# Kernel tuning notes

Hardware: AMD Instinct MI355X
Metric: run time of the kernel (lower is better)

The kernel has to match this reference:

```python
import jax, jax.numpy as jnp
import numpy as np

N_NODES = 100000
N_EDGES = 1200000
D_FEAT = 64
D_OUT = 128


def setup_inputs() -> dict:
    key = jax.random.key(0)
    k1, k2, k3, k4, k5, k6 = jax.random.split(key, 6)
    hk = jax.random.normal(k1, (N_NODES, D_FEAT), dtype=jnp.float32)
    hu = jax.random.normal(k2, (N_NODES, D_FEAT), dtype=jnp.float32)
    W = jax.random.normal(k3, (D_OUT, D_FEAT), dtype=jnp.float32) * 0.05
    b = jax.random.normal(k4, (D_OUT,), dtype=jnp.float32) * 0.05
    src = jax.random.randint(k5, (N_EDGES,), 0, N_NODES, dtype=jnp.int64)
    dst = jax.random.randint(k6, (N_EDGES,), 0, N_NODES, dtype=jnp.int64)
    return {"hk": hk, "hu": hu, "W": W, "b": b, "src": src, "dst": dst}


def reference(hk, hu, W, b, src, dst):
    n = hk.shape[0]
    # u_dot_v: per-edge score = <hk[src], hu[dst]>  -> [E]
    scores = jnp.sum(hk[src] * hu[dst], axis=-1)
    # edge_softmax: softmax over edges grouped by destination node
    seg_max = jax.ops.segment_max(scores, dst, num_segments=n)  # [N]
    ex = jnp.exp(scores - seg_max[dst])                          # [E]
    seg_sum = jax.ops.segment_sum(ex, dst, num_segments=n)      # [N]
    alpha = ex / seg_sum[dst]                                    # [E]
    # u_mul_e_sum: weighted scatter-aggregate of source features into dst
    rst = jax.ops.segment_sum(hk[src] * alpha[:, None], dst, num_segments=n)  # [N, D]
    # fc + relu
    return jax.nn.relu(rst @ W.T + b)
```

## Files before the change

### kernel.cpp

```cpp
#include <hip/hip_runtime.h>
#include <math.h>

#define D_FEAT 64
#define D_OUT  128

__global__ void k_count(const int* __restrict__ dst, int* __restrict__ deg, int E) {
    int e = blockIdx.x * blockDim.x + threadIdx.x;
    if (e >= E) return;
    atomicAdd(deg + dst[e], 1);
}

__global__ __launch_bounds__(256) void k_scan_a(const int* __restrict__ deg,
                                                int* __restrict__ rowptr,
                                                int* __restrict__ partials, int N) {
    __shared__ int wsum[4];
    const int t = threadIdx.x;
    const int base = blockIdx.x * 1024 + t * 4;
    int v0 = (base + 0 < N) ? deg[base + 0] : 0;
    int v1 = (base + 1 < N) ? deg[base + 1] : 0;
    int v2 = (base + 2 < N) ? deg[base + 2] : 0;
    int v3 = (base + 3 < N) ? deg[base + 3] : 0;
    int lsum = v0 + v1 + v2 + v3;
    int x = lsum;
#pragma unroll
    for (int off = 1; off < 64; off <<= 1) {
        int y = __shfl_up(x, off);
        if ((t & 63) >= off) x += y;
    }
    const int wid = t >> 6;
    if ((t & 63) == 63) wsum[wid] = x;
    __syncthreads();
    int woff = 0;
    for (int w = 0; w < wid; ++w) woff += wsum[w];
    int run = woff + x - lsum;
    if (base + 0 < N) rowptr[base + 0] = run; run += v0;
    if (base + 1 < N) rowptr[base + 1] = run; run += v1;
    if (base + 2 < N) rowptr[base + 2] = run; run += v2;
    if (base + 3 < N) rowptr[base + 3] = run;
    if (t == 0) partials[blockIdx.x] = wsum[0] + wsum[1] + wsum[2] + wsum[3];
}

__global__ __launch_bounds__(128) void k_scan_b(int* __restrict__ partials, int NB) {
    __shared__ int buf[128];
    const int t = threadIdx.x;
    const int orig = (t < NB) ? partials[t] : 0;
    buf[t] = orig;
    __syncthreads();
#pragma unroll
    for (int off = 1; off < 128; off <<= 1) {
        int v = (t >= off) ? buf[t - off] : 0;
        __syncthreads();
        buf[t] += v;
        __syncthreads();
    }
    if (t < NB) partials[t] = buf[t] - orig;
}

__global__ __launch_bounds__(256) void k_scan_c(int* __restrict__ rowptr,
                                                int* __restrict__ cursor,
                                                const int* __restrict__ partials,
                                                int N, int E) {
    const int t = threadIdx.x;
    const int base = blockIdx.x * 1024 + t * 4;
    const int add = partials[blockIdx.x];
#pragma unroll
    for (int i = 0; i < 4; ++i) {
        if (base + i < N) {
            int v = rowptr[base + i] + add;
            rowptr[base + i] = v;
            cursor[base + i] = v;
        }
    }
    if (blockIdx.x == 0 && t == 0) rowptr[N] = E;
}

__global__ __launch_bounds__(256) void k_fill(const int* __restrict__ src,
                                              const int* __restrict__ dst,
                                              int* __restrict__ cursor,
                                              int* __restrict__ srcs,
                                              int E, int N) {
    const int pid = (int)(blockIdx.x & 7);
    const int cb  = (int)(blockIdx.x >> 3);
    const int cpp = (int)(gridDim.x >> 3);
    const int lo = (int)(((long long)pid * N) / 8);
    const int hi = (int)(((long long)(pid + 1) * N) / 8);

    const int nq = E >> 2;
    const int stride = cpp * 256;
    for (int q = cb * 256 + (int)threadIdx.x; q < nq; q += stride) {
        const int4 d4 = reinterpret_cast<const int4*>(dst)[q];
        const int e0 = q * 4;
        if (d4.x >= lo && d4.x < hi) { int pos = atomicAdd(cursor + d4.x, 1); srcs[pos] = src[e0 + 0]; }
        if (d4.y >= lo && d4.y < hi) { int pos = atomicAdd(cursor + d4.y, 1); srcs[pos] = src[e0 + 1]; }
        if (d4.z >= lo && d4.z < hi) { int pos = atomicAdd(cursor + d4.z, 1); srcs[pos] = src[e0 + 2]; }
        if (d4.w >= lo && d4.w < hi) { int pos = atomicAdd(cursor + d4.w, 1); srcs[pos] = src[e0 + 3]; }
    }
    if (cb == 0 && (int)threadIdx.x < (E & 3)) {
        int e = nq * 4 + (int)threadIdx.x;
        int d = dst[e];
        if (d >= lo && d < hi) { int pos = atomicAdd(cursor + d, 1); srcs[pos] = src[e]; }
    }
}

__global__ __launch_bounds__(256) void k_agg(const float* __restrict__ hk,
                                             const float* __restrict__ hu,
                                             const int* __restrict__ rowptr,
                                             const int* __restrict__ srcs,
                                             float* __restrict__ rst, int N) {
    const int tid = blockIdx.x * blockDim.x + threadIdx.x;
    const int n = tid >> 6;
    if (n >= N) return;
    const int lane = tid & 63;
    const int q = lane & 15;
    const int g = lane >> 4;

    const int beg = rowptr[n];
    const int end = rowptr[n + 1];

    const float4 hv = *reinterpret_cast<const float4*>(hu + (size_t)n * D_FEAT + q * 4);

    float s = 0.f;
    float4 acc = make_float4(0.f, 0.f, 0.f, 0.f);

    auto process = [&](const float4& a) {
        float dsc = a.x * hv.x + a.y * hv.y + a.z * hv.z + a.w * hv.w;
        dsc += __shfl_xor(dsc, 1);
        dsc += __shfl_xor(dsc, 2);
        dsc += __shfl_xor(dsc, 4);
        dsc += __shfl_xor(dsc, 8);
        const float pe = __expf(fmaxf(fminf(dsc, 80.f), -80.f));
        s += pe;
        acc.x += pe * a.x;
        acc.y += pe * a.y;
        acc.z += pe * a.z;
        acc.w += pe * a.w;
    };

    int p = beg + g;
    if (p < end) {
        float4 a = *reinterpret_cast<const float4*>(hk + (size_t)srcs[p] * D_FEAT + q * 4);
        for (p += 4; p < end; p += 4) {
            const float4 a2 = *reinterpret_cast<const float4*>(hk + (size_t)srcs[p] * D_FEAT + q * 4);
            process(a);
            a = a2;
        }
        process(a);
    }

#pragma unroll
    for (int off = 16; off <= 32; off <<= 1) {
        s     += __shfl_xor(s, off);
        acc.x += __shfl_xor(acc.x, off);
        acc.y += __shfl_xor(acc.y, off);
        acc.z += __shfl_xor(acc.z, off);
        acc.w += __shfl_xor(acc.w, off);
    }

    if (g == 0) {
        float4 o;
        if (end > beg) {
            const float inv = 1.f / s;
            o = make_float4(acc.x * inv, acc.y * inv, acc.z * inv, acc.w * inv);
        } else {
            o = make_float4(0.f, 0.f, 0.f, 0.f);
        }
        *reinterpret_cast<float4*>(rst + (size_t)n * D_FEAT + q * 4) = o;
    }
}

__global__ __launch_bounds__(64) void k_fc(const float* __restrict__ rst,
                                           const float* __restrict__ W,
                                           const float* __restrict__ b,
                                           float* __restrict__ out, int N) {
    __shared__ float lds[64 * 33];
    const int lane = (int)threadIdx.x;
    const int n0 = (int)(blockIdx.x >> 2) * 64;
    const int o0 = (int)(blockIdx.x & 3) * 32;
    const int n = n0 + lane;

    float4 r[16];
    if (n < N) {
        const float4* rp = reinterpret_cast<const float4*>(rst + (size_t)n * D_FEAT);
#pragma unroll
        for (int i = 0; i < 16; ++i) r[i] = rp[i];
    } else {
#pragma unroll
        for (int i = 0; i < 16; ++i) r[i] = make_float4(0.f, 0.f, 0.f, 0.f);
    }

#pragma unroll
    for (int g = 0; g < 8; ++g) {
        const int o = o0 + g * 4;
        const float* w0 = W + (size_t)o * D_FEAT;
        const float* w1 = w0 + D_FEAT;
        const float* w2 = w0 + 2 * D_FEAT;
        const float* w3 = w0 + 3 * D_FEAT;
        float a0 = b[o + 0];
        float a1 = b[o + 1];
        float a2 = b[o + 2];
        float a3 = b[o + 3];
#pragma unroll
        for (int k4 = 0; k4 < 16; ++k4) {
            const float4 rv = r[k4];
            const int k = k4 * 4;
            a0 += rv.x * w0[k] + rv.y * w0[k + 1] + rv.z * w0[k + 2] + rv.w * w0[k + 3];
            a1 += rv.x * w1[k] + rv.y * w1[k + 1] + rv.z * w1[k + 2] + rv.w * w1[k + 3];
            a2 += rv.x * w2[k] + rv.y * w2[k + 1] + rv.z * w2[k + 2] + rv.w * w2[k + 3];
            a3 += rv.x * w3[k] + rv.y * w3[k + 1] + rv.z * w3[k + 2] + rv.w * w3[k + 3];
        }
        lds[lane * 33 + g * 4 + 0] = fmaxf(a0, 0.f);
        lds[lane * 33 + g * 4 + 1] = fmaxf(a1, 0.f);
        lds[lane * 33 + g * 4 + 2] = fmaxf(a2, 0.f);
        lds[lane * 33 + g * 4 + 3] = fmaxf(a3, 0.f);
    }
    __syncthreads();

    const int rrow = lane >> 3;
    const int c = (lane & 7) * 4;
#pragma unroll
    for (int j = 0; j < 8; ++j) {
        const int rr = j * 8 + rrow;
        const int nn = n0 + rr;
        if (nn < N) {
            const float* lp = lds + rr * 33 + c;
            float4 v = make_float4(lp[0], lp[1], lp[2], lp[3]);
            *reinterpret_cast<float4*>(out + (size_t)nn * D_OUT + o0 + c) = v;
        }
    }
}

extern "C" void kernel_launch(void* const* d_in, const int* in_sizes, int n_in,
                              void* d_out, int out_size, void* d_ws, size_t ws_size,
                              hipStream_t stream) {
    const float* hk = (const float*)d_in[0];
    const float* hu = (const float*)d_in[1];
    const float* W  = (const float*)d_in[2];
    const float* b  = (const float*)d_in[3];
    const int* src  = (const int*)d_in[4];
    const int* dst  = (const int*)d_in[5];

    const int N = in_sizes[0] / D_FEAT;
    const int E = in_sizes[4];

    auto pad16 = [](size_t x) { return (x + 15) & ~(size_t)15; };
    size_t o_rowptr = 0;
    size_t o_deg    = pad16(o_rowptr + N + 1);
    size_t o_cursor = o_deg + pad16(N);
    size_t o_srcs   = o_cursor + pad16(N);
    size_t o_part   = o_srcs + pad16(E);
    size_t o_rst    = o_part + 128;

    int* rowptr   = (int*)d_ws + o_rowptr;
    int* deg      = (int*)d_ws + o_deg;
    int* cursor   = (int*)d_ws + o_cursor;
    int* srcs     = (int*)d_ws + o_srcs;
    int* partials = (int*)d_ws + o_part;
    float* rst    = (float*)d_ws + o_rst;

    hipMemsetAsync(deg, 0, pad16(N) * sizeof(int), stream);

    const int B = 256;
    const int g_edge = (E + B - 1) / B;
    const int NB = (N + 1023) / 1024;

    k_count<<<g_edge, B, 0, stream>>>(dst, deg, E);
    k_scan_a<<<NB, 256, 0, stream>>>(deg, rowptr, partials, N);
    k_scan_b<<<1, 128, 0, stream>>>(partials, NB);
    k_scan_c<<<NB, 256, 0, stream>>>(rowptr, cursor, partials, N, E);
    k_fill<<<2048, 256, 0, stream>>>(src, dst, cursor, srcs, E, N);
    k_agg<<<(N + 3) / 4, 256, 0, stream>>>(hk, hu, rowptr, srcs, rst, N);
    k_fc<<<((N + 63) / 64) * 4, 64, 0, stream>>>(rst, W, b, (float*)d_out, N);
}
```

Before: 308.6 us.

## Use bf16 MFMA for the final linear layer and store aggregates as bf16

The aggregation kernel now writes its normalized output as bf16 instead of fp32, and a small kernel converts W to bf16. The fc kernel is rewritten to use 16x16x32 bf16 MFMA instructions in place of scalar FMAs. This halves the intermediate traffic and moves the matmul onto matrix cores. In exchange the GEMM inputs lose precision, and the output stores are strided scalar writes rather than float4.

```diff
diff --git a/kernel.cpp b/kernel.cpp
--- a/kernel.cpp
+++ b/kernel.cpp
@@ -3,6 +3,15 @@
 
 #define D_FEAT 64
 #define D_OUT  128
+
+typedef __attribute__((ext_vector_type(8))) short bf16x8;
+typedef __attribute__((ext_vector_type(4))) float f32x4;
+
+__device__ __forceinline__ unsigned short f2bf(float f) {
+    unsigned u = __float_as_uint(f);
+    unsigned r = (u + 0x7FFFu + ((u >> 16) & 1u)) >> 16;
+    return (unsigned short)r;
+}
 
 __global__ void k_count(const int* __restrict__ dst, int* __restrict__ deg, int E) {
     int e = blockIdx.x * blockDim.x + threadIdx.x;
@@ -106,7 +115,7 @@
                                              const float* __restrict__ hu,
                                              const int* __restrict__ rowptr,
                                              const int* __restrict__ srcs,
-                                             float* __restrict__ rst, int N) {
+                                             unsigned short* __restrict__ rst_bf, int N) {
     const int tid = blockIdx.x * blockDim.x + threadIdx.x;
     const int n = tid >> 6;
     if (n >= N) return;
@@ -157,74 +166,78 @@
     }
 
     if (g == 0) {
-        float4 o;
+        ushort4 o;
         if (end > beg) {
             const float inv = 1.f / s;
-            o = make_float4(acc.x * inv, acc.y * inv, acc.z * inv, acc.w * inv);
+            o.x = f2bf(acc.x * inv);
+            o.y = f2bf(acc.y * inv);
+            o.z = f2bf(acc.z * inv);
+            o.w = f2bf(acc.w * inv);
         } else {
-            o = make_float4(0.f, 0.f, 0.f, 0.f);
-        }
-        *reinterpret_cast<float4*>(rst + (size_t)n * D_FEAT + q * 4) = o;
-    }
-}
-
-__global__ __launch_bounds__(64) void k_fc(const float* __restrict__ rst,
-                                           const float* __restrict__ W,
-                                           const float* __restrict__ b,
-                                           float* __restrict__ out, int N) {
-    __shared__ float lds[64 * 33];
-    const int lane = (int)threadIdx.x;
-    const int n0 = (int)(blockIdx.x >> 2) * 64;
-    const int o0 = (int)(blockIdx.x & 3) * 32;
-    const int n = n0 + lane;
-
-    float4 r[16];
-    if (n < N) {
-        const float4* rp = reinterpret_cast<const float4*>(rst + (size_t)n * D_FEAT);
-#pragma unroll
-        for (int i = 0; i < 16; ++i) r[i] = rp[i];
+            o.x = o.y = o.z = o.w = 0;
+        }
+        *reinterpret_cast<ushort4*>(rst_bf + (size_t)n * D_FEAT + q * 4) = o;
+    }
+}
+
+__global__ __launch_bounds__(256) void k_wcvt(const float* __restrict__ W,
+                                              unsigned short* __restrict__ Wbf) {
+    const int i = (blockIdx.x * 256 + threadIdx.x) * 4;
+    const float4 w = *reinterpret_cast<const float4*>(W + i);
+    ushort4 o;
+    o.x = f2bf(w.x); o.y = f2bf(w.y); o.z = f2bf(w.z); o.w = f2bf(w.w);
+    *reinterpret_cast<ushort4*>(Wbf + i) = o;
+}
+
+__global__ __launch_bounds__(256) void k_fc(const unsigned short* __restrict__ rst_bf,
+                                            const unsigned short* __restrict__ Wbf,
+                                            const float* __restrict__ bias,
+                                            float* __restrict__ out, int N) {
+    const int l   = (int)(threadIdx.x & 63);
+    const int wv  = (int)(threadIdx.x >> 6);
+    const int c16 = l & 15;
+    const int kg  = l >> 4;
+    const int n0  = (int)blockIdx.x * 64 + wv * 16;
+
+    bf16x8 bf[8][2];
+#pragma unroll
+    for (int t = 0; t < 8; ++t) {
+#pragma unroll
+        for (int kh = 0; kh < 2; ++kh) {
+            bf[t][kh] = *reinterpret_cast<const bf16x8*>(
+                Wbf + (size_t)(t * 16 + c16) * D_FEAT + kh * 32 + kg * 8);
+        }
+    }
+
+    const int na = n0 + c16;
+    bf16x8 af[2];
+    if (na < N) {
+#pragma unroll
+        for (int kh = 0; kh < 2; ++kh) {
+            af[kh] = *reinterpret_cast<const bf16x8*>(
+                rst_bf + (size_t)na * D_FEAT + kh * 32 + kg * 8);
+        }
     } else {
-#pragma unroll
-        for (int i = 0; i < 16; ++i) r[i] = make_float4(0.f, 0.f, 0.f, 0.f);
-    }
-
-#pragma unroll
-    for (int g = 0; g < 8; ++g) {
-        const int o = o0 + g * 4;
-        const float* w0 = W + (size_t)o * D_FEAT;
-        const float* w1 = w0 + D_FEAT;
-        const float* w2 = w0 + 2 * D_FEAT;
-        const float* w3 = w0 + 3 * D_FEAT;
-        float a0 = b[o + 0];
-        float a1 = b[o + 1];
-        float a2 = b[o + 2];
-        float a3 = b[o + 3];
-#pragma unroll
-        for (int k4 = 0; k4 < 16; ++k4) {
-            const float4 rv = r[k4];
-            const int k = k4 * 4;
-            a0 += rv.x * w0[k] + rv.y * w0[k + 1] + rv.z * w0[k + 2] + rv.w * w0[k + 3];
-            a1 += rv.x * w1[k] + rv.y * w1[k + 1] + rv.z * w1[k + 2] + rv.w * w1[k + 3];
-            a2 += rv.x * w2[k] + rv.y * w2[k + 1] + rv.z * w2[k + 2] + rv.w * w2[k + 3];
-            a3 += rv.x * w3[k] + rv.y * w3[k + 1] + rv.z * w3[k + 2] + rv.w * w3[k + 3];
-        }
-        lds[lane * 33 + g * 4 + 0] = fmaxf(a0, 0.f);
-        lds[lane * 33 + g * 4 + 1] = fmaxf(a1, 0.f);
-        lds[lane * 33 + g * 4 + 2] = fmaxf(a2, 0.f);
-        lds[lane * 33 + g * 4 + 3] = fmaxf(a3, 0.f);
-    }
-    __syncthreads();
-
-    const int rrow = lane >> 3;
-    const int c = (lane & 7) * 4;
-#pragma unroll
-    for (int j = 0; j < 8; ++j) {
-        const int rr = j * 8 + rrow;
-        const int nn = n0 + rr;
-        if (nn < N) {
-            const float* lp = lds + rr * 33 + c;
-            float4 v = make_float4(lp[0], lp[1], lp[2], lp[3]);
-            *reinterpret_cast<float4*>(out + (size_t)nn * D_OUT + o0 + c) = v;
+        af[0] = (bf16x8)0;
+        af[1] = (bf16x8)0;
+    }
+
+    f32x4 acc[8];
+#pragma unroll
+    for (int t = 0; t < 8; ++t) {
+        f32x4 z = {0.f, 0.f, 0.f, 0.f};
+        z = __builtin_amdgcn_mfma_f32_16x16x32_bf16(af[0], bf[t][0], z, 0, 0, 0);
+        acc[t] = __builtin_amdgcn_mfma_f32_16x16x32_bf16(af[1], bf[t][1], z, 0, 0, 0);
+    }
+
+#pragma unroll
+    for (int t = 0; t < 8; ++t) {
+        const float bv = bias[t * 16 + c16];
+#pragma unroll
+        for (int r = 0; r < 4; ++r) {
+            const int nn = n0 + kg * 4 + r;
+            if (nn < N)
+                out[(size_t)nn * D_OUT + t * 16 + c16] = fmaxf(acc[t][r] + bv, 0.f);
         }
     }
 }
@@ -248,14 +261,16 @@
     size_t o_cursor = o_deg + pad16(N);
     size_t o_srcs   = o_cursor + pad16(N);
     size_t o_part   = o_srcs + pad16(E);
-    size_t o_rst    = o_part + 128;
+    size_t o_rstbf  = pad16(o_part + 128);
+    size_t o_wbf    = o_rstbf + pad16((size_t)N * 32);
 
     int* rowptr   = (int*)d_ws + o_rowptr;
     int* deg      = (int*)d_ws + o_deg;
     int* cursor   = (int*)d_ws + o_cursor;
     int* srcs     = (int*)d_ws + o_srcs;
     int* partials = (int*)d_ws + o_part;
-    float* rst    = (float*)d_ws + o_rst;
+    unsigned short* rst_bf = (unsigned short*)((int*)d_ws + o_rstbf);
+    unsigned short* Wbf    = (unsigned short*)((int*)d_ws + o_wbf);
 
     hipMemsetAsync(deg, 0, pad16(N) * sizeof(int), stream);
 
@@ -263,11 +278,12 @@
     const int g_edge = (E + B - 1) / B;
     const int NB = (N + 1023) / 1024;
 
+    k_wcvt<<<(D_OUT * D_FEAT) / (256 * 4), 256, 0, stream>>>(W, Wbf);
     k_count<<<g_edge, B, 0, stream>>>(dst, deg, E);
     k_scan_a<<<NB, 256, 0, stream>>>(deg, rowptr, partials, N);
     k_scan_b<<<1, 128, 0, stream>>>(partials, NB);
     k_scan_c<<<NB, 256, 0, stream>>>(rowptr, cursor, partials, N, E);
     k_fill<<<2048, 256, 0, stream>>>(src, dst, cursor, srcs, E, N);
-    k_agg<<<(N + 3) / 4, 256, 0, stream>>>(hk, hu, rowptr, srcs, rst, N);
-    k_fc<<<((N + 63) / 64) * 4, 64, 0, stream>>>(rst, W, b, (float*)d_out, N);
-}
+    k_agg<<<(N + 3) / 4, 256, 0, stream>>>(hk, hu, rowptr, srcs, rst_bf, N);
+    k_fc<<<(N + 63) / 64, 256, 0, stream>>>(rst_bf, Wbf, b, (float*)d_out, N);
+}
```

Result: faster. 290.1 us (-6.0%).
